# Optimization experiments

Measured on AMD Instinct MI355X. Metric: run time of the kernel, lower is better.

Reference implementation:

```python
import jax, jax.numpy as jnp
import numpy as np

N, K, D, G = 6000, 300, 1024, 16
DG = D // G          # 64 per-head dim
EMB = 64             # position embedding feat_dim


def setup_inputs():
    key = jax.random.key(0)
    ks = jax.random.split(key, 8)
    merged_feat = jax.random.normal(ks[0], (N, D), dtype=jnp.float32)
    u = jax.random.uniform(ks[1], (N, 4), dtype=jnp.float32)
    x1 = u[:, 0] * 800.0
    y1 = u[:, 1] * 800.0
    bboxes = jnp.stack([x1, y1, x1 + u[:, 2] * 200.0 + 8.0, y1 + u[:, 3] * 200.0 + 8.0], axis=1)
    s = 0.02
    Wq = jax.random.normal(ks[2], (D, D), dtype=jnp.float32) * s
    Wk = jax.random.normal(ks[3], (D, D), dtype=jnp.float32) * s
    Wg = jax.random.normal(ks[4], (G, EMB), dtype=jnp.float32) * s
    Wv = jax.random.normal(ks[5], (G, DG, D), dtype=jnp.float32) * s
    bq = jnp.zeros((D,), jnp.float32)
    bk = jnp.zeros((D,), jnp.float32)
    bg = jnp.zeros((G,), jnp.float32)
    bv = jnp.zeros((D,), jnp.float32)
    return dict(merged_feat=merged_feat, bboxes=bboxes, Wq=Wq, bq=bq, Wk=Wk, bk=bk,
                Wg=Wg, bg=bg, Wv=Wv, bv=bv, k=K)


def _cdist(x, y):
    # torch.cdist(p=2): sqrt of clamped squared distances
    sq = jnp.sum(x * x, 1)[:, None] + jnp.sum(y * y, 1)[None, :] - 2.0 * (x @ y.T)
    return jnp.sqrt(jnp.maximum(sq, 0.0))


def _fps_greedy(feat, k):
    # select_farthest_k_sequential: greedy lowest-redundancy sampling on 1/cdist
    Drec = 1.0 / _cdist(feat, feat)  # diagonal -> inf, never argmin-selected

    def step(ds, _):
        idx = jnp.argmin(ds)
        return ds + Drec[idx], idx

    _, rest = jax.lax.scan(step, Drec[0], None, length=k - 1)
    return jnp.concatenate([jnp.zeros((1,), rest.dtype), rest])


def _pos_embedding(bbox, ref_bbox):
    # extract_position_matrix + extract_position_embedding(feat_dim=64)
    xmin, ymin, xmax, ymax = jnp.split(ref_bbox, 4, axis=1)
    wr = xmax - xmin + 1.0
    hr = ymax - ymin + 1.0
    cxr = 0.5 * (xmin + xmax)
    cyr = 0.5 * (ymin + ymax)
    xmin, ymin, xmax, ymax = jnp.split(bbox, 4, axis=1)
    w = xmax - xmin + 1.0
    h = ymax - ymin + 1.0
    cx = 0.5 * (xmin + xmax)
    cy = 0.5 * (ymin + ymax)
    dx = jnp.log(jnp.abs((cx - cxr.T) / w) + 1e-3)
    dy = jnp.log(jnp.abs((cy - cyr.T) / h) + 1e-3)
    dw = jnp.log(w / wr.T)
    dh = jnp.log(h / hr.T)
    pos = jnp.stack([dx, dy, dw, dh], axis=2)            # (k, N, 4)
    rng = jnp.arange(EMB // 8, dtype=jnp.float32)         # 8 frequencies
    dim_mat = jnp.power(1000.0, (8.0 / EMB) * rng)        # (8,)
    div = pos[..., None] * 100.0 / dim_mat               # (k, N, 4, 8)
    emb = jnp.concatenate([jnp.sin(div), jnp.cos(div)], axis=3)  # (k, N, 4, 16)
    return emb.reshape(emb.shape[0], emb.shape[1], EMB)   # (k, N, 64)


def _attention(roi_feat, ref_feat, pos_emb, Wq, bq, Wk, bk, Wg, bg, Wv, bv):
    # attention_module_multi_head: position-gated multi-head relation attention
    k = roi_feat.shape[0]
    # Wgs 1x1 conv (64 -> 16 groups), relu, -> aff_weight (k, G, N)
    aff_weight = jax.nn.relu(jnp.einsum('ge,kne->kgn', Wg, pos_emb) + bg[None, :, None])
    q = (roi_feat @ Wq.T + bq).reshape(k, G, DG)          # (k, G, 64)
    kk = (ref_feat @ Wk.T + bk).reshape(-1, G, DG)        # (N, G, 64)
    aff = jnp.einsum('kgd,ngd->kgn', q, kk) * (1.0 / np.sqrt(float(DG)))
    weighted = jnp.log(aff_weight + 1e-6) + aff
    soft = jax.nn.softmax(weighted, axis=2)               # (k, G, N)
    out_t = jnp.einsum('kgn,nd->kgd', soft, ref_feat)     # (k, G, D)
    # Wvs grouped 1x1 conv (G*D -> D, groups=G)
    return jnp.einsum('kgc,goc->kgo', out_t, Wv).reshape(k, D) + bv


def reference(merged_feat, bboxes, Wq, bq, Wk, bk, Wg, bg, Wv, bv, k):
    idx = _fps_greedy(merged_feat, k)
    roi_feat = merged_feat[idx]
    pos_emb = _pos_embedding(bboxes[idx], bboxes)
    return _attention(roi_feat, merged_feat, pos_emb, Wq, bq, Wk, bk, Wg, bg, Wv, bv)
```

## Files before the change

kernel.cpp:

```cpp
#include <hip/hip_runtime.h>
#include <math.h>

#define N_PTS 6000
#define DIM   1024
#define KSEL  300
#define GG    16
#define DGR   64
#define WSTR  6016
#define XSTR  2048

typedef _Float16 half8 __attribute__((ext_vector_type(8)));
typedef float floatx4 __attribute__((ext_vector_type(4)));

__device__ __forceinline__ unsigned short f2h(float x) {
    _Float16 h = (_Float16)x;
    return __builtin_bit_cast(unsigned short, h);
}
__device__ __forceinline__ float h2f(unsigned short u) {
    return (float)__builtin_bit_cast(_Float16, u);
}

__device__ __forceinline__ void async_copy16(const void* gsrc, void* ldst) {
    __builtin_amdgcn_global_load_lds(
        (const __attribute__((address_space(1))) void*)gsrc,
        (__attribute__((address_space(3))) void*)ldst,
        16, 0, 0);
}

template<bool GRAM, bool OF16>
__global__ __launch_bounds__(256)
void mfma_gemm(const void* Av, long lda, long az,
               const void* Bv, long ldb, long bz,
               void* Cv, long ldc, long cz,
               int M, int N, int Kd,
               const float* __restrict__ bias, long biasz,
               float scale, const float* __restrict__ sqn, int nbm)
{
    __shared__ unsigned short As[128 * 32];
    __shared__ unsigned short Bs[128 * 32];
    const int t = threadIdx.x;
    const int w = t >> 6, l = t & 63;
    const int wr = w >> 1, wc = w & 1;

    int row0, col0, bi = 0, bj = 0;
    if (GRAM) {
        int tt = blockIdx.x, rem = nbm;
        while (tt >= rem) { tt -= rem; bi++; rem--; }
        bj = bi + tt;
        row0 = bi * 128; col0 = bj * 128;
    } else {
        row0 = blockIdx.y * 128; col0 = blockIdx.x * 128;
    }
    const int z = blockIdx.z;
    const unsigned short* Ab = (const unsigned short*)Av + (long)z * az;
    const unsigned short* Bb = (const unsigned short*)Bv + (long)z * bz;

    floatx4 acc[4][4];
#pragma unroll
    for (int i = 0; i < 4; i++)
#pragma unroll
        for (int j = 0; j < 4; j++) acc[i][j] = (floatx4){0.f, 0.f, 0.f, 0.f};

    int ra0 = row0 + (w * 2 + 0) * 16 + (l >> 2); ra0 = ra0 < M ? ra0 : M - 1;
    int ra1 = row0 + (w * 2 + 1) * 16 + (l >> 2); ra1 = ra1 < M ? ra1 : M - 1;
    int rb0 = col0 + (w * 2 + 0) * 16 + (l >> 2); rb0 = rb0 < N ? rb0 : N - 1;
    int rb1 = col0 + (w * 2 + 1) * 16 + (l >> 2); rb1 = rb1 < N ? rb1 : N - 1;
    const long lane_off = (l & 3) * 8;
    const unsigned short* gA0 = Ab + (long)ra0 * lda + lane_off;
    const unsigned short* gA1 = Ab + (long)ra1 * lda + lane_off;
    const unsigned short* gB0 = Bb + (long)rb0 * ldb + lane_off;
    const unsigned short* gB1 = Bb + (long)rb1 * ldb + lane_off;
    unsigned short* lA0 = As + ((w * 2 + 0) * 16) * 32;
    unsigned short* lA1 = As + ((w * 2 + 1) * 16) * 32;
    unsigned short* lB0 = Bs + ((w * 2 + 0) * 16) * 32;
    unsigned short* lB1 = Bs + ((w * 2 + 1) * 16) * 32;

    auto kstep = [&](long offA, long offB) {
        async_copy16(gA0 + offA, (void*)lA0);
        async_copy16(gA1 + offA, (void*)lA1);
        async_copy16(gB0 + offB, (void*)lB0);
        async_copy16(gB1 + offB, (void*)lB1);
        __syncthreads();
        half8 af[4], bfr[4];
#pragma unroll
        for (int ti = 0; ti < 4; ti++)
            af[ti] = *(const half8*)(As + (wr * 64 + ti * 16 + (l & 15)) * 32 + (l >> 4) * 8);
#pragma unroll
        for (int tj = 0; tj < 4; tj++)
            bfr[tj] = *(const half8*)(Bs + (wc * 64 + tj * 16 + (l & 15)) * 32 + (l >> 4) * 8);
#pragma unroll
        for (int ti = 0; ti < 4; ti++)
#pragma unroll
            for (int tj = 0; tj < 4; tj++)
                acc[ti][tj] = __builtin_amdgcn_mfma_f32_16x16x32_f16(
                    af[ti], bfr[tj], acc[ti][tj], 0, 0, 0);
        __syncthreads();
    };

    if (GRAM) {
#pragma unroll 1
        for (int k0 = 0; k0 < 1024; k0 += 32) kstep(k0, k0);
#pragma unroll 1
        for (int k0 = 0; k0 < 1024; k0 += 32) kstep(k0, k0 + 1024);
#pragma unroll 1
        for (int k0 = 0; k0 < 1024; k0 += 32) kstep(k0 + 1024, k0);
    } else {
#pragma unroll 1
        for (int k0 = 0; k0 < Kd; k0 += 32) kstep(k0, k0);
    }

    float* Cf = (float*)Cv + (long)z * cz;
    unsigned short* Ch = (unsigned short*)Cv + (long)z * cz;
    const float* bias_p = bias ? bias + (long)z * biasz : nullptr;
#pragma unroll
    for (int ti = 0; ti < 4; ti++) {
#pragma unroll
        for (int tj = 0; tj < 4; tj++) {
            const int c = col0 + wc * 64 + tj * 16 + (l & 15);
            const int rb = row0 + wr * 64 + ti * 16 + (l >> 4) * 4;
            if (GRAM) {
                float rec4[4];
#pragma unroll
                for (int reg = 0; reg < 4; reg++) {
                    int r = rb + reg;
                    if (r >= M || c >= N) { rec4[reg] = 0.f; continue; }
                    if (r == c) { rec4[reg] = INFINITY; }
                    else {
                        float sq = sqn[r] + sqn[c] - 2.f * acc[ti][tj][reg];
                        rec4[reg] = 1.0f / sqrtf(fmaxf(sq, 0.f));
                    }
                    Cf[(long)r * ldc + c] = rec4[reg];
                }
                if (bi != bj && c < N && rb + 3 < M) {
                    *(float4*)(Cf + (long)c * ldc + rb) =
                        make_float4(rec4[0], rec4[1], rec4[2], rec4[3]);
                }
            } else {
#pragma unroll
                for (int reg = 0; reg < 4; reg++) {
                    int r = rb + reg;
                    if (r >= M || c >= N) continue;
                    float v = acc[ti][tj][reg] * scale;
                    if (bias_p) v += bias_p[c];
                    if (OF16) Ch[(long)r * ldc + c] = f2h(v);
                    else      Cf[(long)r * ldc + c] = v;
                }
            }
        }
    }
}

#define BM 128
#define BN 128
#define BKK 8
#define TM 8
#define TN 8

template<bool TRANSB>
__global__ __launch_bounds__(256)
void sgemm_kernel(const float* __restrict__ A, long lda, long az,
                  const float* __restrict__ B, long ldb, long bz,
                  float* __restrict__ C, long ldc, long cz,
                  int M, int N, int Kd,
                  const float* __restrict__ bias, long biasz, float scale)
{
    __shared__ float As[BKK][BM];
    __shared__ float Bs[BKK][BN];
    const int t = threadIdx.x;
    const int z = blockIdx.z;
    A += (long)z * az; B += (long)z * bz; C += (long)z * cz;
    const float* bias_p = bias ? (bias + (long)z * biasz) : nullptr;
    const int row0 = blockIdx.y * BM;
    const int col0 = blockIdx.x * BN;
    const int tx = t & 15, ty = t >> 4;

    float acc[TM][TN];
#pragma unroll
    for (int i = 0; i < TM; i++)
#pragma unroll
        for (int j = 0; j < TN; j++) acc[i][j] = 0.f;

    const int lrow = t >> 1;
    const int lcol = (t & 1) * 4;

    for (int k0 = 0; k0 < Kd; k0 += BKK) {
        {
            int r = row0 + lrow; r = (r < M) ? r : (M - 1);
            float4 v = *(const float4*)(A + (long)r * lda + (k0 + lcol));
            As[lcol + 0][lrow] = v.x; As[lcol + 1][lrow] = v.y;
            As[lcol + 2][lrow] = v.z; As[lcol + 3][lrow] = v.w;
        }
        {
            int r = col0 + lrow; r = (r < N) ? r : (N - 1);
            float4 v = *(const float4*)(B + (long)r * ldb + (k0 + lcol));
            Bs[lcol + 0][lrow] = v.x; Bs[lcol + 1][lrow] = v.y;
            Bs[lcol + 2][lrow] = v.z; Bs[lcol + 3][lrow] = v.w;
        }
        __syncthreads();
#pragma unroll
        for (int kk = 0; kk < BKK; kk++) {
            float a[TM], b[TN];
#pragma unroll
            for (int i = 0; i < TM; i++) a[i] = As[kk][ty * TM + i];
#pragma unroll
            for (int j = 0; j < TN; j++) b[j] = Bs[kk][tx * TN + j];
#pragma unroll
            for (int i = 0; i < TM; i++)
#pragma unroll
                for (int j = 0; j < TN; j++)
                    acc[i][j] = fmaf(a[i], b[j], acc[i][j]);
        }
        __syncthreads();
    }
#pragma unroll
    for (int i = 0; i < TM; i++) {
        int r = row0 + ty * TM + i;
        if (r >= M) continue;
#pragma unroll
        for (int j = 0; j < TN; j++) {
            int c = col0 + tx * TN + j;
            if (c >= N) continue;
            float v = acc[i][j] * scale;
            if (bias_p) v += bias_p[c];
            C[(long)r * ldc + c] = v;
        }
    }
}

__global__ __launch_bounds__(256)
void sqnpack2_kernel(const float* __restrict__ feat,
                     unsigned short* __restrict__ X, float* __restrict__ sqn)
{
    const int r = blockIdx.x, t = threadIdx.x;
    float4 v = *(const float4*)(feat + (long)r * DIM + t * 4);
    float s = v.x * v.x + v.y * v.y + v.z * v.z + v.w * v.w;

    ushort4 hi, lo;
    hi.x = f2h(v.x); lo.x = f2h(v.x - h2f(hi.x));
    hi.y = f2h(v.y); lo.y = f2h(v.y - h2f(hi.y));
    hi.z = f2h(v.z); lo.z = f2h(v.z - h2f(hi.z));
    hi.w = f2h(v.w); lo.w = f2h(v.w - h2f(hi.w));
    *(ushort4*)(X + (long)r * XSTR + t * 4) = hi;
    *(ushort4*)(X + (long)r * XSTR + 1024 + t * 4) = lo;

#pragma unroll
    for (int o = 32; o > 0; o >>= 1) s += __shfl_down(s, o);
    __shared__ float sr[4];
    if ((t & 63) == 0) sr[t >> 6] = s;
    __syncthreads();
    if (t == 0) sqn[r] = sr[0] + sr[1] + sr[2] + sr[3];
}

__global__ __launch_bounds__(256)
void wconv2_kernel(const float* __restrict__ Wq, const float* __restrict__ Wk,
                   unsigned short* __restrict__ Wq_h, unsigned short* __restrict__ Wk_h)
{
    const int b = blockIdx.x;
    const float* src = (b < 1024) ? Wq : Wk;
    unsigned short* dst = (b < 1024) ? Wq_h : Wk_h;
    const long i = ((long)(b & 1023) * 256 + threadIdx.x) * 4;
    float4 v = *(const float4*)(src + i);
    ushort4 o;
    o.x = f2h(v.x); o.y = f2h(v.y); o.z = f2h(v.z); o.w = f2h(v.w);
    *(ushort4*)(dst + i) = o;
}

__global__ __launch_bounds__(256)
void transpose_kernel(const float* __restrict__ feat, unsigned short* __restrict__ featT)
{
    __shared__ unsigned short tile[32][33];
    const int bx = blockIdx.x;
    const int by = blockIdx.y;
    const int t = threadIdx.x;
    const int lr = t >> 3;
    const int lc = (t & 7) * 4;
    const int r = by * 32 + lr;
    if (r < N_PTS) {
        float4 v = *(const float4*)(feat + (long)r * DIM + bx * 32 + lc);
        tile[lr][lc + 0] = f2h(v.x); tile[lr][lc + 1] = f2h(v.y);
        tile[lr][lc + 2] = f2h(v.z); tile[lr][lc + 3] = f2h(v.w);
    } else {
        tile[lr][lc + 0] = 0; tile[lr][lc + 1] = 0;
        tile[lr][lc + 2] = 0; tile[lr][lc + 3] = 0;
    }
    __syncthreads();
    const int orow = bx * 32 + lr;
    ushort4 o;
    o.x = tile[lc + 0][lr]; o.y = tile[lc + 1][lr];
    o.z = tile[lc + 2][lr]; o.w = tile[lc + 3][lr];
    *(ushort4*)(featT + (long)orow * WSTR + by * 32 + lc) = o;
}

#define FPS_T 1024

__global__ __launch_bounds__(1024)
void fps_kernel(const float* __restrict__ Drec, int* __restrict__ idxout)
{
    const int t = threadIdx.x;
    const bool act = t < 750;
    float ds[8];
    if (act) {
        const float4* p = (const float4*)Drec + 2 * t;
        float4 a0 = p[0], a1 = p[1];
        ds[0] = a0.x; ds[1] = a0.y; ds[2] = a0.z; ds[3] = a0.w;
        ds[4] = a1.x; ds[5] = a1.y; ds[6] = a1.z; ds[7] = a1.w;
    } else {
#pragma unroll
        for (int j = 0; j < 8; j++) ds[j] = INFINITY;
    }
    __shared__ unsigned long long red[16];
    __shared__ int s_sel;
    if (t == 0) idxout[0] = 0;

    for (int it = 1; it < KSEL; it++) {
        float mv = ds[0]; int mi = 8 * t;
#pragma unroll
        for (int j = 1; j < 8; j++) {
            if (ds[j] < mv) { mv = ds[j]; mi = 8 * t + j; }
        }
        unsigned long long key = act
            ? (((unsigned long long)__float_as_uint(mv) << 32) | (unsigned)mi)
            : ~0ull;
#pragma unroll
        for (int o = 32; o > 0; o >>= 1) {
            unsigned long long other = __shfl_down(key, o);
            if (other < key) key = other;
        }
        if ((t & 63) == 0) red[t >> 6] = key;
        __syncthreads();
        if (t < 64) {
            unsigned long long k2 = (t < 16) ? red[t] : ~0ull;
#pragma unroll
            for (int o = 8; o > 0; o >>= 1) {
                unsigned long long other = __shfl_down(k2, o);
                if (other < k2) k2 = other;
            }
            if (t == 0) s_sel = (int)(unsigned)(k2 & 0xffffffffull);
        }
        __syncthreads();
        const int sel = s_sel;
        if (t == 0) idxout[it] = sel;
        if (act) {
            const float4* rp = (const float4*)(Drec + (long)sel * N_PTS) + 2 * t;
            float4 r0 = rp[0], r1 = rp[1];
            ds[0] += r0.x; ds[1] += r0.y; ds[2] += r0.z; ds[3] += r0.w;
            ds[4] += r1.x; ds[5] += r1.y; ds[6] += r1.z; ds[7] += r1.w;
        }
    }
}

__global__ __launch_bounds__(256)
void gatherb_kernel(const unsigned short* __restrict__ X, const int* __restrict__ idx,
                    unsigned short* __restrict__ roi)
{
    const int k = blockIdx.x, t = threadIdx.x;
    const unsigned short* src = X + (long)idx[k] * XSTR;
    *(ushort4*)(roi + (long)k * DIM + t * 4) = *(const ushort4*)(src + t * 4);
}

__global__ __launch_bounds__(256)
void gatelogit_kernel(const float* __restrict__ bboxes,
                      const int* __restrict__ idx,
                      const float* __restrict__ Wg,
                      const float* __restrict__ bgp,
                      float* __restrict__ W)
{
    __shared__ float swg[GG][64];
    __shared__ float sbg[GG];
    __shared__ float sbb[4];
    const int t = threadIdx.x;
    const int k = blockIdx.y;
    const int n = blockIdx.x * 256 + t;
    for (int i = t; i < GG * 64; i += 256) swg[i >> 6][i & 63] = Wg[i];
    if (t < GG) sbg[t] = bgp[t];
    if (t < 4)  sbb[t] = bboxes[(long)idx[k] * 4 + t];
    __syncthreads();
    if (n >= N_PTS) return;

    const float x1 = sbb[0], y1 = sbb[1], x2 = sbb[2], y2 = sbb[3];
    const float w  = x2 - x1 + 1.f, h = y2 - y1 + 1.f;
    const float cx = 0.5f * (x1 + x2), cy = 0.5f * (y1 + y2);
    float4 rb = *(const float4*)(bboxes + (long)n * 4);
    const float wr = rb.z - rb.x + 1.f, hr = rb.w - rb.y + 1.f;
    const float cxr = 0.5f * (rb.x + rb.z), cyr = 0.5f * (rb.y + rb.w);

    float pos[4];
    pos[0] = __logf(fabsf((cx - cxr) / w) + 1e-3f);
    pos[1] = __logf(fabsf((cy - cyr) / h) + 1e-3f);
    pos[2] = __logf(w / wr);
    pos[3] = __logf(h / hr);

    const float rdm[8] = { 100.0f, 42.169650342858226f, 17.782794100389228f,
                           7.498942093324559f, 3.1622776601683795f,
                           1.333521432163324f, 0.5623413251903491f,
                           0.23713737056616552f };
    float aw[GG];
#pragma unroll
    for (int g = 0; g < GG; g++) aw[g] = sbg[g];
#pragma unroll
    for (int p = 0; p < 4; p++) {
#pragma unroll
        for (int f = 0; f < 8; f++) {
            const float arg = pos[p] * rdm[f];
            const float s_ = __sinf(arg), c_ = __cosf(arg);
            const int e = p * 16 + f;
#pragma unroll
            for (int g = 0; g < GG; g++)
                aw[g] += swg[g][e] * s_ + swg[g][e + 8] * c_;
        }
    }
    float* base = W + ((long)k * GG) * WSTR + n;
#pragma unroll
    for (int g = 0; g < GG; g++) {
        const float lg = __logf(fmaxf(aw[g], 0.f) + 1e-6f);
        base[(long)g * WSTR] += lg;
    }
}

__global__ __launch_bounds__(256)
void softmax16_kernel(float* __restrict__ W)
{
    __shared__ float lg[WSTR];
    __shared__ float sred[4];
    __shared__ float sMS;
    const int t = threadIdx.x;
    float* rowp = W + (long)blockIdx.x * WSTR;

    float m = -INFINITY;
    for (int n = t; n < N_PTS; n += 256) {
        const float v = rowp[n];
        lg[n] = v;
        m = fmaxf(m, v);
    }
#pragma unroll
    for (int o = 32; o > 0; o >>= 1) m = fmaxf(m, __shfl_down(m, o));
    if ((t & 63) == 0) sred[t >> 6] = m;
    __syncthreads();
    if (t == 0) sMS = fmaxf(fmaxf(sred[0], sred[1]), fmaxf(sred[2], sred[3]));
    __syncthreads();
    m = sMS;
    __syncthreads();

    float s = 0.f;
    for (int n = t; n < N_PTS; n += 256) {
        const float e = __expf(lg[n] - m);
        lg[n] = e;
        s += e;
    }
#pragma unroll
    for (int o = 32; o > 0; o >>= 1) s += __shfl_down(s, o);
    if ((t & 63) == 0) sred[t >> 6] = s;
    __syncthreads();
    if (t == 0) sMS = sred[0] + sred[1] + sred[2] + sred[3];
    __syncthreads();
    const float inv = 1.0f / sMS;
    __syncthreads();

    unsigned short* orow = (unsigned short*)rowp;
    for (int n = t; n < WSTR; n += 256)
        orow[n] = (n < N_PTS) ? f2h(lg[n] * inv) : (unsigned short)0;
}

extern "C" void kernel_launch(void* const* d_in, const int* in_sizes, int n_in,
                              void* d_out, int out_size, void* d_ws, size_t ws_size,
                              hipStream_t stream)
{
    const float* feat   = (const float*)d_in[0];
    const float* bboxes = (const float*)d_in[1];
    const float* Wq     = (const float*)d_in[2];
    const float* bq     = (const float*)d_in[3];
    const float* Wk     = (const float*)d_in[4];
    const float* bk     = (const float*)d_in[5];
    const float* Wg     = (const float*)d_in[6];
    const float* bg     = (const float*)d_in[7];
    const float* Wv     = (const float*)d_in[8];
    const float* bv     = (const float*)d_in[9];
    float* out = (float*)d_out;
    float* ws  = (float*)d_ws;

    float* drec = ws;
    float* W    = ws;
    unsigned short* kk_h  = (unsigned short*)(ws + 28900000);
    unsigned short* q_h   = (unsigned short*)(ws + 31972000);
    unsigned short* roi_h = (unsigned short*)(ws + 32125600);
    unsigned short* featT = (unsigned short*)(ws + 32300000);
    unsigned short* X     = (unsigned short*)(ws + 36000000);
    float* outt           = ws + 36000000;
    unsigned short* Wq_h  = (unsigned short*)(ws + 45216000);
    unsigned short* Wk_h  = (unsigned short*)(ws + 45740288);
    float* sqnbuf         = ws + 46264576;
    int*   idxbuf         = (int*)(ws + 46270576);
    if (ws_size < (size_t)185100000) return;

    sqnpack2_kernel<<<N_PTS, 256, 0, stream>>>(feat, X, sqnbuf);
    wconv2_kernel<<<2048, 256, 0, stream>>>(Wq, Wk, Wq_h, Wk_h);

    mfma_gemm<true, false><<<1128, 256, 0, stream>>>(
        X, XSTR, 0, X, XSTR, 0, drec, N_PTS, 0,
        N_PTS, N_PTS, 3072, nullptr, 0, 1.f, sqnbuf, 47);

    fps_kernel<<<1, FPS_T, 0, stream>>>(drec, idxbuf);

    transpose_kernel<<<dim3(32, 188), 256, 0, stream>>>(feat, featT);
    gatherb_kernel<<<KSEL, 256, 0, stream>>>(X, idxbuf, roi_h);

    mfma_gemm<false, true><<<dim3(8, 3, 1), 256, 0, stream>>>(
        roi_h, 1024, 0, Wq_h, 1024, 0, q_h, 1024, 0,
        KSEL, DIM, DIM, bq, 0, 1.f, nullptr, 0);
    mfma_gemm<false, true><<<dim3(8, 47, 1), 256, 0, stream>>>(
        X, XSTR, 0, Wk_h, 1024, 0, kk_h, 1024, 0,
        N_PTS, DIM, DIM, bk, 0, 1.f, nullptr, 0);

    mfma_gemm<false, false><<<dim3(47, 3, GG), 256, 0, stream>>>(
        q_h, 1024, 64, kk_h, 1024, 64, W, (long)GG * WSTR, WSTR,
        KSEL, N_PTS, 64, nullptr, 0, 0.125f, nullptr, 0);

    gatelogit_kernel<<<dim3(24, KSEL), 256, 0, stream>>>(
        bboxes, idxbuf, Wg, bg, W);
    softmax16_kernel<<<KSEL * GG, 256, 0, stream>>>(W);

    mfma_gemm<false, false><<<dim3(8, 38, 1), 256, 0, stream>>>(
        (unsigned short*)W, 2 * WSTR, 0, featT, WSTR, 0, outt, DIM, 0,
        KSEL * GG, DIM, WSTR, nullptr, 0, 1.f, nullptr, 0);

    sgemm_kernel<true><<<dim3(1, 3, GG), 256, 0, stream>>>(
        outt, (long)GG * DIM, DIM, Wv, DIM, (long)DGR * DIM, out, DIM, DGR,
        KSEL, DGR, DIM, bv, DGR, 1.f);
}
```

Before: 1.227 ms.

## Fuse K projection GEMM into FPS launch to overlap with serial selection

Launches the single-block greedy farthest-point selection together with 96 extra blocks that compute the K projection GEMM in the same kernel. The GEMM runs on otherwise idle compute units while the serial FPS loop executes. The kk buffer is moved out of the distance-matrix region to avoid clobbering data FPS is still reading. The trade-off is a specialised GEMM copy and extra contention for memory bandwidth during FPS.

Result: no change. 1.211 ms (-1.3%).

```diff
diff --git a/kernel.cpp b/kernel.cpp
--- a/kernel.cpp
+++ b/kernel.cpp
@@ -150,6 +150,145 @@
     }
 }
 
+#define FPS_T 1024
+
+__global__ __launch_bounds__(1024)
+void fps_kk_kernel(const float* __restrict__ Drec, int* __restrict__ idxout,
+                   const unsigned short* __restrict__ X,
+                   const unsigned short* __restrict__ Wk_h,
+                   const float* __restrict__ bk,
+                   unsigned short* __restrict__ kk_h)
+{
+    __shared__ unsigned long long red[16];
+    __shared__ int s_sel;
+    __shared__ unsigned short As[4][128 * 32];
+    __shared__ unsigned short Bs[128 * 32];
+    const int t = threadIdx.x;
+
+    if (blockIdx.x == 0) {
+        const bool act = t < 750;
+        float ds[8];
+        if (act) {
+            const float4* p = (const float4*)Drec + 2 * t;
+            float4 a0 = p[0], a1 = p[1];
+            ds[0] = a0.x; ds[1] = a0.y; ds[2] = a0.z; ds[3] = a0.w;
+            ds[4] = a1.x; ds[5] = a1.y; ds[6] = a1.z; ds[7] = a1.w;
+        } else {
+#pragma unroll
+            for (int j = 0; j < 8; j++) ds[j] = INFINITY;
+        }
+        if (t == 0) idxout[0] = 0;
+
+        for (int it = 1; it < KSEL; it++) {
+            float mv = ds[0]; int mi = 8 * t;
+#pragma unroll
+            for (int j = 1; j < 8; j++) {
+                if (ds[j] < mv) { mv = ds[j]; mi = 8 * t + j; }
+            }
+            unsigned long long key = act
+                ? (((unsigned long long)__float_as_uint(mv) << 32) | (unsigned)mi)
+                : ~0ull;
+#pragma unroll
+            for (int o = 32; o > 0; o >>= 1) {
+                unsigned long long other = __shfl_down(key, o);
+                if (other < key) key = other;
+            }
+            if ((t & 63) == 0) red[t >> 6] = key;
+            __syncthreads();
+            if (t < 64) {
+                unsigned long long k2 = (t < 16) ? red[t] : ~0ull;
+#pragma unroll
+                for (int o = 8; o > 0; o >>= 1) {
+                    unsigned long long other = __shfl_down(k2, o);
+                    if (other < k2) k2 = other;
+                }
+                if (t == 0) s_sel = (int)(unsigned)(k2 & 0xffffffffull);
+            }
+            __syncthreads();
+            const int sel = s_sel;
+            if (t == 0) idxout[it] = sel;
+            if (act) {
+                const float4* rp = (const float4*)(Drec + (long)sel * N_PTS) + 2 * t;
+                float4 r0 = rp[0], r1 = rp[1];
+                ds[0] += r0.x; ds[1] += r0.y; ds[2] += r0.z; ds[3] += r0.w;
+                ds[4] += r1.x; ds[5] += r1.y; ds[6] += r1.z; ds[7] += r1.w;
+            }
+        }
+        return;
+    }
+
+    const int b = blockIdx.x - 1;
+    const int mg = b >> 3;
+    const int nt = b & 7;
+    const int w = t >> 6, l = t & 63;
+    const int sub = w >> 2;
+    const int wsu = w & 3;
+    const int wr = wsu >> 1, wc = wsu & 1;
+    const int row0 = (mg * 4 + sub) * 128;
+    const int col0 = nt * 128;
+
+    floatx4 acc[4][4];
+#pragma unroll
+    for (int i = 0; i < 4; i++)
+#pragma unroll
+        for (int j = 0; j < 4; j++) acc[i][j] = (floatx4){0.f, 0.f, 0.f, 0.f};
+
+    int ra0 = row0 + (wsu * 2 + 0) * 16 + (l >> 2); ra0 = ra0 < N_PTS ? ra0 : N_PTS - 1;
+    int ra1 = row0 + (wsu * 2 + 1) * 16 + (l >> 2); ra1 = ra1 < N_PTS ? ra1 : N_PTS - 1;
+    const long lane_off = (l & 3) * 8;
+    const unsigned short* gA0 = X + (long)ra0 * XSTR + lane_off;
+    const unsigned short* gA1 = X + (long)ra1 * XSTR + lane_off;
+    unsigned short* lA0 = As[sub] + ((wsu * 2 + 0) * 16) * 32;
+    unsigned short* lA1 = As[sub] + ((wsu * 2 + 1) * 16) * 32;
+    const int rb0 = col0 + (wsu * 2 + 0) * 16 + (l >> 2);
+    const int rb1 = col0 + (wsu * 2 + 1) * 16 + (l >> 2);
+    const unsigned short* gB0 = Wk_h + (long)rb0 * DIM + lane_off;
+    const unsigned short* gB1 = Wk_h + (long)rb1 * DIM + lane_off;
+    unsigned short* lB0 = Bs + ((wsu * 2 + 0) * 16) * 32;
+    unsigned short* lB1 = Bs + ((wsu * 2 + 1) * 16) * 32;
+
+#pragma unroll 1
+    for (int k0 = 0; k0 < DIM; k0 += 32) {
+        async_copy16(gA0 + k0, (void*)lA0);
+        async_copy16(gA1 + k0, (void*)lA1);
+        if (sub == 0) {
+            async_copy16(gB0 + k0, (void*)lB0);
+            async_copy16(gB1 + k0, (void*)lB1);
+        }
+        __syncthreads();
+        half8 af[4], bfr[4];
+#pragma unroll
+        for (int ti = 0; ti < 4; ti++)
+            af[ti] = *(const half8*)(As[sub] + (wr * 64 + ti * 16 + (l & 15)) * 32 + (l >> 4) * 8);
+#pragma unroll
+        for (int tj = 0; tj < 4; tj++)
+            bfr[tj] = *(const half8*)(Bs + (wc * 64 + tj * 16 + (l & 15)) * 32 + (l >> 4) * 8);
+#pragma unroll
+        for (int ti = 0; ti < 4; ti++)
+#pragma unroll
+            for (int tj = 0; tj < 4; tj++)
+                acc[ti][tj] = __builtin_amdgcn_mfma_f32_16x16x32_f16(
+                    af[ti], bfr[tj], acc[ti][tj], 0, 0, 0);
+        __syncthreads();
+    }
+
+#pragma unroll
+    for (int ti = 0; ti < 4; ti++) {
+#pragma unroll
+        for (int tj = 0; tj < 4; tj++) {
+            const int c = col0 + wc * 64 + tj * 16 + (l & 15);
+            const int rbase = row0 + wr * 64 + ti * 16 + (l >> 4) * 4;
+            const float bkc = bk[c];
+#pragma unroll
+            for (int reg = 0; reg < 4; reg++) {
+                const int r = rbase + reg;
+                if (r < N_PTS)
+                    kk_h[(long)r * DIM + c] = f2h(acc[ti][tj][reg] + bkc);
+            }
+        }
+    }
+}
+
 #define BM 128
 #define BN 128
 #define BKK 8
@@ -291,64 +430,6 @@
     *(ushort4*)(featT + (long)orow * WSTR + by * 32 + lc) = o;
 }
 
-#define FPS_T 1024
-
-__global__ __launch_bounds__(1024)
-void fps_kernel(const float* __restrict__ Drec, int* __restrict__ idxout)
-{
-    const int t = threadIdx.x;
-    const bool act = t < 750;
-    float ds[8];
-    if (act) {
-        const float4* p = (const float4*)Drec + 2 * t;
-        float4 a0 = p[0], a1 = p[1];
-        ds[0] = a0.x; ds[1] = a0.y; ds[2] = a0.z; ds[3] = a0.w;
-        ds[4] = a1.x; ds[5] = a1.y; ds[6] = a1.z; ds[7] = a1.w;
-    } else {
-#pragma unroll
-        for (int j = 0; j < 8; j++) ds[j] = INFINITY;
-    }
-    __shared__ unsigned long long red[16];
-    __shared__ int s_sel;
-    if (t == 0) idxout[0] = 0;
-
-    for (int it = 1; it < KSEL; it++) {
-        float mv = ds[0]; int mi = 8 * t;
-#pragma unroll
-        for (int j = 1; j < 8; j++) {
-            if (ds[j] < mv) { mv = ds[j]; mi = 8 * t + j; }
-        }
-        unsigned long long key = act
-            ? (((unsigned long long)__float_as_uint(mv) << 32) | (unsigned)mi)
-            : ~0ull;
-#pragma unroll
-        for (int o = 32; o > 0; o >>= 1) {
-            unsigned long long other = __shfl_down(key, o);
-            if (other < key) key = other;
-        }
-        if ((t & 63) == 0) red[t >> 6] = key;
-        __syncthreads();
-        if (t < 64) {
-            unsigned long long k2 = (t < 16) ? red[t] : ~0ull;
-#pragma unroll
-            for (int o = 8; o > 0; o >>= 1) {
-                unsigned long long other = __shfl_down(k2, o);
-                if (other < k2) k2 = other;
-            }
-            if (t == 0) s_sel = (int)(unsigned)(k2 & 0xffffffffull);
-        }
-        __syncthreads();
-        const int sel = s_sel;
-        if (t == 0) idxout[it] = sel;
-        if (act) {
-            const float4* rp = (const float4*)(Drec + (long)sel * N_PTS) + 2 * t;
-            float4 r0 = rp[0], r1 = rp[1];
-            ds[0] += r0.x; ds[1] += r0.y; ds[2] += r0.z; ds[3] += r0.w;
-            ds[4] += r1.x; ds[5] += r1.y; ds[6] += r1.z; ds[7] += r1.w;
-        }
-    }
-}
-
 __global__ __launch_bounds__(256)
 void gatherb_kernel(const unsigned short* __restrict__ X, const int* __restrict__ idx,
                     unsigned short* __restrict__ roi)
@@ -480,12 +561,12 @@
 
     float* drec = ws;
     float* W    = ws;
-    unsigned short* kk_h  = (unsigned short*)(ws + 28900000);
     unsigned short* q_h   = (unsigned short*)(ws + 31972000);
     unsigned short* roi_h = (unsigned short*)(ws + 32125600);
     unsigned short* featT = (unsigned short*)(ws + 32300000);
     unsigned short* X     = (unsigned short*)(ws + 36000000);
     float* outt           = ws + 36000000;
+    unsigned short* kk_h  = (unsigned short*)(ws + 42144000);
     unsigned short* Wq_h  = (unsigned short*)(ws + 45216000);
     unsigned short* Wk_h  = (unsigned short*)(ws + 45740288);
     float* sqnbuf         = ws + 46264576;
@@ -499,7 +580,7 @@
         X, XSTR, 0, X, XSTR, 0, drec, N_PTS, 0,
         N_PTS, N_PTS, 3072, nullptr, 0, 1.f, sqnbuf, 47);
 
-    fps_kernel<<<1, FPS_T, 0, stream>>>(drec, idxbuf);
+    fps_kk_kernel<<<97, 1024, 0, stream>>>(drec, idxbuf, X, Wk_h, bk, kk_h);
 
     transpose_kernel<<<dim3(32, 188), 256, 0, stream>>>(feat, featT);
     gatherb_kernel<<<KSEL, 256, 0, stream>>>(X, idxbuf, roi_h);
@@ -507,9 +588,6 @@
     mfma_gemm<false, true><<<dim3(8, 3, 1), 256, 0, stream>>>(
         roi_h, 1024, 0, Wq_h, 1024, 0, q_h, 1024, 0,
         KSEL, DIM, DIM, bq, 0, 1.f, nullptr, 0);
-    mfma_gemm<false, true><<<dim3(8, 47, 1), 256, 0, stream>>>(
-        X, XSTR, 0, Wk_h, 1024, 0, kk_h, 1024, 0,
-        N_PTS, DIM, DIM, bk, 0, 1.f, nullptr, 0);
 
     mfma_gemm<false, false><<<dim3(47, 3, GG), 256, 0, stream>>>(
         q_h, 1024, 64, kk_h, 1024, 64, W, (long)GG * WSTR, WSTR,
```
